# Kernel tuning notes

Hardware: AMD Instinct MI355X
Metric: run time of the kernel (lower is better)

Reference implementation:

```python
import jax, jax.numpy as jnp
import numpy as np

B, S, D, H = 4, 2048, 256, 8  # batch, seq (context=target), hidden_dim, n_heads


def setup_inputs() -> dict:
    key = jax.random.key(0)
    ks = jax.random.split(key, 12)
    sd = 1.0 / np.sqrt(D)          # torch Linear default init scale (uniform bound)
    sdo = 1.0 / np.sqrt(H * D)
    inp = {
        "k": jax.random.normal(ks[0], (B, S, D), jnp.float32),
        "v": jax.random.normal(ks[1], (B, S, D), jnp.float32),
        "q": jax.random.normal(ks[2], (B, S, D), jnp.float32),
        # Per-head projection weights, stacked over heads. Stored so y = x @ W + b.
        "Wk": jax.random.uniform(ks[3], (H, D, D), jnp.float32, -sd, sd),
        "bk": jax.random.uniform(ks[4], (H, D), jnp.float32, -sd, sd),
        "Wv": jax.random.uniform(ks[5], (H, D, D), jnp.float32, -sd, sd),
        "bv": jax.random.uniform(ks[6], (H, D), jnp.float32, -sd, sd),
        "Wq": jax.random.uniform(ks[7], (H, D, D), jnp.float32, -sd, sd),
        "bq": jax.random.uniform(ks[8], (H, D), jnp.float32, -sd, sd),
        # Final mixing Linear: input is heads interleaved as (hidden, head) flattened,
        # i.e. input index = hid * H + head (torch stack(dim=-1).view order).
        "Wo": jax.random.uniform(ks[9], (H * D, D), jnp.float32, -sdo, sdo),
        "bo": jax.random.uniform(ks[10], (D,), jnp.float32, -sdo, sdo),
    }
    return inp


def reference(k, v, q, Wk, bk, Wv, bv, Wq, bq, Wo, bo):
    # Per-head linear projections (batched over heads instead of a Python loop)
    k_ = jnp.einsum('bmd,hde->bhme', k, Wk) + bk[None, :, None, :]  # [B,H,S,D]
    v_ = jnp.einsum('bmd,hde->bhme', v, Wv) + bv[None, :, None, :]
    q_ = jnp.einsum('bnd,hde->bhne', q, Wq) + bq[None, :, None, :]
    scale = jnp.asarray(np.sqrt(D), k.dtype)
    # dot attention: scores[b,h,n,m] = <q_n, k_m> / sqrt(D); softmax over keys m
    scores = jnp.einsum('bhnd,bhmd->bhnm', q_, k_) / scale
    w = jax.nn.softmax(scores, axis=-1)
    rep = jnp.einsum('bhnm,bhmd->bhnd', w, v_)  # [B,H,S,D]
    # torch: stack(heads, dim=-1) -> [B,S,D,H], then view -> [B,S,D*H] (hid-major)
    outs = rep.transpose(0, 2, 3, 1).reshape(rep.shape[0], rep.shape[2], -1)
    return outs @ Wo + bo
```

## Files before the change

kernel.cpp:

```cpp
#include <hip/hip_runtime.h>

#define BB 4
#define SS 2048
#define DD 256
#define HH 8

typedef unsigned short u16;
typedef __attribute__((ext_vector_type(8))) short bf16x8;
typedef __attribute__((ext_vector_type(4))) float f32x4;
typedef __attribute__((ext_vector_type(16))) float f32x16;
typedef __attribute__((ext_vector_type(4))) short s16x4;

__device__ __forceinline__ f32x4 MFMA(bf16x8 a, bf16x8 b, f32x4 c) {
    return __builtin_amdgcn_mfma_f32_16x16x32_bf16(a, b, c, 0, 0, 0);
}
__device__ __forceinline__ f32x16 MFMA32(bf16x8 a, bf16x8 b, f32x16 c) {
    return __builtin_amdgcn_mfma_f32_32x32x16_bf16(a, b, c, 0, 0, 0);
}

__device__ __forceinline__ u16 f2bf_rtn(float x) {
    unsigned u = __float_as_uint(x);
    u += 0x7FFFu + ((u >> 16) & 1u);
    return (u16)(u >> 16);
}
__device__ __forceinline__ float bf2f(u16 h) {
    return __uint_as_float(((unsigned)h) << 16);
}
__device__ __forceinline__ void split2(float x, u16 &hi, u16 &lo) {
    hi = f2bf_rtn(x);
    lo = f2bf_rtn(x - bf2f(hi));
}

__device__ __forceinline__ void gl_lds16(const u16* g, u16* l) {
    __builtin_amdgcn_global_load_lds(
        (const __attribute__((address_space(1))) unsigned int*)(g),
        (__attribute__((address_space(3))) unsigned int*)(l), 16, 0, 0);
}

__global__ void prep_a(const float* __restrict__ x, u16* __restrict__ hi) {
    int r = blockIdx.x;
    int d = threadIdx.x;
    hi[(size_t)r * 256 + d] = f2bf_rtn(x[(size_t)r * 256 + d]);
}

__global__ void prep_w(const float* __restrict__ W, u16* __restrict__ Whi,
                       u16* __restrict__ Wlo) {
    int n = blockIdx.x;
    int h = n >> 8, e = n & 255;
    int d = threadIdx.x;
    float x = W[((size_t)h * 256 + d) * 256 + e];
    u16 hi, lo; split2(x, hi, lo);
    Whi[(size_t)n * 256 + d] = hi;
    Wlo[(size_t)n * 256 + d] = lo;
}

__global__ void prep_wo(const float* __restrict__ W, u16* __restrict__ Whi,
                        u16* __restrict__ Wlo) {
    int n = blockIdx.x;
    for (int k = threadIdx.x; k < 2048; k += 256) {
        int d = k & 255, h = k >> 8;
        float x = W[((size_t)(d * 8 + h)) * 256 + n];
        u16 hi, lo; split2(x, hi, lo);
        Whi[(size_t)n * 2048 + k] = hi;
        Wlo[(size_t)n * 2048 + k] = lo;
    }
}

__global__ void reduce_out(const float* __restrict__ P, const float* __restrict__ bias,
                           float* __restrict__ out) {
    const int i = blockIdx.x * 1024 + threadIdx.x * 4;
    f32x4 a = *(const f32x4*)(P + i);
    f32x4 b = *(const f32x4*)(P + 2097152 + i);
    f32x4 bv = *(const f32x4*)(bias + ((threadIdx.x * 4) & 255));
    *(f32x4*)(out + i) = (a + b) + bv;
}

template<int MODE, int AMODE, int TERMS, int BN, int LNXB, int SPLK>
__global__ __launch_bounds__(512, 2) void gemm_split(
    const u16* __restrict__ Ahi, const u16* __restrict__ Alo,
    const u16* __restrict__ Bhi, const u16* __restrict__ Blo,
    const float* __restrict__ bias,
    u16* __restrict__ Ohi,
    float* __restrict__ Of,
    int M, int N, int K, float scale)
{
    constexpr int WN = (BN == 128) ? 4 : 2;
    constexpr int WM = 8 / WN;
    constexpr int MSUB = (128 / WM) / 16;
    constexpr int NSUB = (BN / WN) / 16;
    constexpr int NPL = (TERMS == 3) ? 4 : (TERMS == 2) ? 3 : 2;
    constexpr int NBUF = SPLK ? 2 : 3;

    __shared__ u16 lds[NBUF * NPL * 4096];

    const int tid = threadIdx.x;
    const int lane = tid & 63, wave = tid >> 6;
    const int wm = wave / WN, wn = wave % WN;
    const int nwg = (int)gridDim.x >> SPLK;
    const int kc = SPLK ? (blockIdx.x >= (unsigned)nwg ? 1 : 0) : 0;
    const int b2 = SPLK ? ((int)blockIdx.x - kc * nwg) : (int)blockIdx.x;
    const int cpx = nwg >> 3;
    const int wgs = (b2 & 7) * cpx + (b2 >> 3);
    const int m0 = (wgs >> LNXB) * 128;
    const int n0 = (wgs & ((1 << LNXB) - 1)) * BN;
    const int kb = kc * (K >> SPLK);

    f32x4 acc[MSUB][NSUB];
#pragma unroll
    for (int i = 0; i < MSUB; ++i)
#pragma unroll
        for (int j = 0; j < NSUB; ++j) acc[i][j] = {0.f, 0.f, 0.f, 0.f};

    const int rho = tid >> 2;
    const int Xs = (tid & 3) << 3;
    const int ldsW = wave * 512;

#define G_ISSUE(k0v, p)                                                         \
    {   u16* Bse = lds + (p) * (NPL * 4096);                                    \
        size_t ga;                                                              \
        if (AMODE == 0)                                                         \
            ga = (size_t)(m0 + rho) * K + (k0v) + Xs;                           \
        else                                                                    \
            ga = ((size_t)((m0 >> 11) * 8 + ((k0v) >> 8)) * SS                  \
                  + (m0 & 2047) + rho) * DD + ((k0v) & 255) + Xs;               \
        gl_lds16(Ahi + ga, Bse + ldsW);                                         \
        if (TERMS == 3) gl_lds16(Alo + ga, Bse + 3 * 4096 + ldsW);              \
        if (BN == 128 || tid < 256) {                                           \
            size_t gb = (size_t)(n0 + rho) * K + (k0v) + Xs;                    \
            gl_lds16(Bhi + gb, Bse + 1 * 4096 + ldsW);                          \
            if (TERMS >= 2) gl_lds16(Blo + gb, Bse + 2 * 4096 + ldsW);          \
        }                                                                       \
    }

    const int NK = (K >> 5) >> SPLK;
    G_ISSUE(kb, 0);
    if (NBUF == 3) G_ISSUE(kb + 32, 1);

    int buf = 0;
    for (int kt = 0; kt < NK; ++kt) {
        if (NBUF == 3) {
            if (kt < NK - 1) {
                if (TERMS == 1)      { asm volatile("s_waitcnt vmcnt(2)" ::: "memory"); }
                else if (TERMS == 2) { asm volatile("s_waitcnt vmcnt(3)" ::: "memory"); }
                else {
                    if (wave < 4) { asm volatile("s_waitcnt vmcnt(4)" ::: "memory"); }
                    else          { asm volatile("s_waitcnt vmcnt(2)" ::: "memory"); }
                }
            } else {
                asm volatile("s_waitcnt vmcnt(0)" ::: "memory");
            }
        } else {
            asm volatile("s_waitcnt vmcnt(0)" ::: "memory");
        }
        __builtin_amdgcn_sched_barrier(0);
        __builtin_amdgcn_s_barrier();
        __builtin_amdgcn_sched_barrier(0);

        if (NBUF == 3) {
            if (kt + 2 < NK) {
                const int p2 = (buf + 2 >= 3) ? buf - 1 : buf + 2;
                G_ISSUE(kb + ((kt + 2) << 5), p2);
            }
        } else {
            if (kt + 1 < NK) G_ISSUE(kb + ((kt + 1) << 5), (kt + 1) & 1);
        }

        const u16* Bse = lds + buf * (NPL * 4096);
        const int g8 = (lane >> 4) << 3;
        const int rA = wm * (128 / WM), rB = wn * (BN / WN);
        bf16x8 bh[NSUB], bl[NSUB];
#pragma unroll
        for (int ns = 0; ns < NSUB; ++ns) {
            const int rb = rB + ns * 16 + (lane & 15);
            bh[ns] = *(const bf16x8*)(Bse + 1 * 4096 + rb * 32 + g8);
            if (TERMS >= 2) bl[ns] = *(const bf16x8*)(Bse + 2 * 4096 + rb * 32 + g8);
        }
#pragma unroll
        for (int ms = 0; ms < MSUB; ++ms) {
            const int ra = rA + ms * 16 + (lane & 15);
            bf16x8 ah = *(const bf16x8*)(Bse + ra * 32 + g8);
            bf16x8 al;
            if (TERMS == 3) al = *(const bf16x8*)(Bse + 3 * 4096 + ra * 32 + g8);
#pragma unroll
            for (int ns = 0; ns < NSUB; ++ns) {
                acc[ms][ns] = MFMA(ah, bh[ns], acc[ms][ns]);
                if (TERMS == 3) acc[ms][ns] = MFMA(al, bh[ns], acc[ms][ns]);
                if (TERMS >= 2) acc[ms][ns] = MFMA(ah, bl[ns], acc[ms][ns]);
            }
        }
        buf = (buf + 1 == NBUF) ? 0 : buf + 1;
    }
#undef G_ISSUE

#pragma unroll
    for (int ms = 0; ms < MSUB; ++ms)
#pragma unroll
        for (int ns = 0; ns < NSUB; ++ns)
#pragma unroll
            for (int r = 0; r < 4; ++r) {
                int row = m0 + wm * (128 / WM) + ms * 16 + (lane >> 4) * 4 + r;
                int col = n0 + wn * (BN / WN) + ns * 16 + (lane & 15);
                if (MODE == 3) {
                    Of[(size_t)kc * ((size_t)M * N) + (size_t)row * N + col] =
                        acc[ms][ns][r];
                } else {
                    float v = (acc[ms][ns][r] + bias[col]) * scale;
                    if (MODE == 2) {
                        Of[(size_t)row * N + col] = v;
                    } else {
                        int b = row >> 11, s = row & 2047, hh = col >> 8, e = col & 255;
                        size_t idx;
                        if (MODE == 0)
                            idx = ((size_t)(b * HH + hh) * SS + s) * DD + e;
                        else
                            idx = ((size_t)(b * HH + hh) * DD + e) * SS + s;
                        Ohi[idx] = f2bf_rtn(v);
                    }
                }
            }
}

__global__ __launch_bounds__(512, 2) void attn_kernel(
    const u16* __restrict__ Qhi,
    const u16* __restrict__ Khi,
    const u16* __restrict__ Vhi,
    u16* __restrict__ Rhi, u16* __restrict__ Rlo)
{
    __shared__ u16 lK[3][8192];
    __shared__ u16 lV[3][8192];

    const int tid = threadIdx.x, lane = tid & 63, wave = tid >> 6;
    const int qc = lane & 31, g2 = lane >> 5;
    const int wg = ((blockIdx.x & 7) << 5) + (blockIdx.x >> 3);
    const int bh = wg >> 3;
    const int qt = wg & 7;
    const size_t base = (size_t)bh * SS * DD;
    const int q0w = qt * 256 + wave * 32;

    bf16x8 qB[16];
#pragma unroll
    for (int ks = 0; ks < 16; ++ks)
        qB[ks] = *(const bf16x8*)(Qhi + base + (size_t)(q0w + qc) * DD + ks * 16 + g2 * 8);

    int koff[2], voff[2];
#pragma unroll
    for (int i = 0; i < 2; ++i) {
        const int s = tid + i * 512;
        const int kr = s >> 5, kX = s & 31;
        const int kap = (kr & 0x13) | ((kr & 4) << 1) | ((kr & 8) >> 1);
        koff[i] = kap * DD + ((kX ^ kr) << 3);
        const int ve = s >> 2, vXs = s & 3;
        voff[i] = ve * SS + (((vXs ^ ((ve >> 3) & 3))) << 3);
    }

    float l_part = 0.f;
    f32x16 acc[8];
#pragma unroll
    for (int ec = 0; ec < 8; ++ec) acc[ec] = {};

#define ISSUE(tt, p)                                                            \
    {   const u16* Kg = Khi + base + (size_t)(tt) * 32 * DD;                    \
        const u16* Vg = Vhi + base + (size_t)(tt) * 32;                         \
        u16* Kb = &lK[p][0]; u16* Vb = &lV[p][0];                               \
        gl_lds16(Kg + koff[0], Kb + wave * 512);                                \
        gl_lds16(Kg + koff[1], Kb + wave * 512 + 4096);                         \
        gl_lds16(Vg + voff[0], Vb + wave * 512);                                \
        gl_lds16(Vg + voff[1], Vb + wave * 512 + 4096);                         \
    }

    ISSUE(0, 0);
    ISSUE(1, 1);

    for (int t = 0; t < 64; ++t) {
        if (t < 63) { asm volatile("s_waitcnt vmcnt(4)" ::: "memory"); }
        else        { asm volatile("s_waitcnt vmcnt(0)" ::: "memory"); }
        __builtin_amdgcn_sched_barrier(0);
        __builtin_amdgcn_s_barrier();
        __builtin_amdgcn_sched_barrier(0);

        if (t + 2 < 64) ISSUE(t + 2, (t + 2) % 3);

        const u16* Kb = &lK[t % 3][0];
        const u16* Vb = &lV[t % 3][0];

        f32x16 sa = {}, sb = {};
        __builtin_amdgcn_s_setprio(1);
#pragma unroll
        for (int ks = 0; ks < 8; ++ks) {
            bf16x8 ka = *(const bf16x8*)(Kb + qc * DD + (((2 * ks + g2) ^ qc) << 3));
            bf16x8 kb2 = *(const bf16x8*)(Kb + qc * DD + (((2 * (ks + 8) + g2) ^ qc) << 3));
            sa = MFMA32(ka, qB[ks], sa);
            sb = MFMA32(kb2, qB[ks + 8], sb);
        }
        __builtin_amdgcn_s_setprio(0);

        f32x16 s = sa + sb;
#pragma unroll
        for (int n = 0; n < 16; ++n) s[n] = __builtin_amdgcn_exp2f(s[n] - 8.0f);
        float tl = 0.f;
#pragma unroll
        for (int n = 0; n < 16; ++n) tl += s[n];
        l_part += tl;

        bf16x8 p0, p1;
#pragma unroll
        for (int j = 0; j < 4; ++j) {
            unsigned a = __float_as_uint(s[2 * j]);
            unsigned b = __float_as_uint(s[2 * j + 1]);
            ((unsigned*)&p0)[j] = (a >> 16) | (b & 0xffff0000u);
            unsigned c = __float_as_uint(s[8 + 2 * j]);
            unsigned d = __float_as_uint(s[8 + 2 * j + 1]);
            ((unsigned*)&p1)[j] = (c >> 16) | (d & 0xffff0000u);
        }

        __builtin_amdgcn_s_setprio(1);
#pragma unroll
        for (int ec = 0; ec < 8; ++ec) {
            const int e = ec * 32 + qc;
            bf16x8 v0 = *(const bf16x8*)(Vb + e * 32 + (((g2 ^ ((e >> 3) & 3))) << 3));
            bf16x8 v1 = *(const bf16x8*)(Vb + e * 32 + ((((2 + g2) ^ ((e >> 3) & 3))) << 3));
            acc[ec] = MFMA32(v0, p0, acc[ec]);
            acc[ec] = MFMA32(v1, p1, acc[ec]);
        }
        __builtin_amdgcn_s_setprio(0);
    }
#undef ISSUE

    float l = l_part + __shfl_xor(l_part, 32);
    float inv = 1.0f / l;
    const size_t rowbase = ((size_t)bh * SS + q0w + qc) * DD;
#pragma unroll
    for (int ec = 0; ec < 8; ++ec)
#pragma unroll
        for (int rr = 0; rr < 4; ++rr) {
            const int e0 = ec * 32 + 8 * rr + 4 * g2;
            s16x4 hv, lv;
#pragma unroll
            for (int j = 0; j < 4; ++j) {
                u16 h2, l2; split2(acc[ec][4 * rr + j] * inv, h2, l2);
                hv[j] = (short)h2; lv[j] = (short)l2;
            }
            *(s16x4*)(Rhi + rowbase + e0) = hv;
            *(s16x4*)(Rlo + rowbase + e0) = lv;
        }
}

extern "C" void kernel_launch(void* const* d_in, const int* in_sizes, int n_in,
                              void* d_out, int out_size, void* d_ws, size_t ws_size,
                              hipStream_t stream)
{
    (void)in_sizes; (void)n_in; (void)out_size; (void)ws_size;
    const float* k_in = (const float*)d_in[0];
    const float* v_in = (const float*)d_in[1];
    const float* q_in = (const float*)d_in[2];
    const float* Wk   = (const float*)d_in[3];
    const float* bk   = (const float*)d_in[4];
    const float* Wv   = (const float*)d_in[5];
    const float* bv   = (const float*)d_in[6];
    const float* Wq   = (const float*)d_in[7];
    const float* bq   = (const float*)d_in[8];
    const float* Wo   = (const float*)d_in[9];
    const float* bo   = (const float*)d_in[10];
    float* out = (float*)d_out;

    char* p = (char*)d_ws;
    const size_t MB = 1024 * 1024;
    u16* WqH = (u16*)(p + 0 * MB);
    u16* WqL = (u16*)(p + 1 * MB);
    u16* WkH = (u16*)(p + 2 * MB);
    u16* WkL = (u16*)(p + 3 * MB);
    u16* WvH = (u16*)(p + 4 * MB);
    u16* WvL = (u16*)(p + 5 * MB);
    u16* WoH = (u16*)(p + 6 * MB);
    u16* WoL = (u16*)(p + 7 * MB);
    const size_t PB = 32 * MB;
    u16* QH  = (u16*)(p + 8 * MB);
    u16* KH  = (u16*)(p + 8 * MB + 1 * PB);
    u16* VTH = (u16*)(p + 8 * MB + 2 * PB);
    u16* RH  = (u16*)(p + 8 * MB + 3 * PB);
    u16* RL  = (u16*)(p + 8 * MB + 4 * PB);
    u16* AqH = (u16*)(p + 168 * MB);
    u16* AkH = (u16*)(p + 172 * MB);
    u16* AvH = (u16*)(p + 176 * MB);
    float* Pf = (float*)(p + 8 * MB);

    prep_a<<<dim3(8192), dim3(256), 0, stream>>>(q_in, AqH);
    prep_a<<<dim3(8192), dim3(256), 0, stream>>>(k_in, AkH);
    prep_a<<<dim3(8192), dim3(256), 0, stream>>>(v_in, AvH);
    prep_w<<<dim3(2048), dim3(256), 0, stream>>>(Wq, WqH, WqL);
    prep_w<<<dim3(2048), dim3(256), 0, stream>>>(Wk, WkH, WkL);
    prep_w<<<dim3(2048), dim3(256), 0, stream>>>(Wv, WvH, WvL);
    prep_wo<<<dim3(256), dim3(256), 0, stream>>>(Wo, WoH, WoL);

    const float qscale = 1.4426950408889634f / 16.0f;
    gemm_split<0, 0, 1, 128, 4, 0><<<dim3(1024), dim3(512), 0, stream>>>(
        AqH, nullptr, WqH, WqL, bq, QH, nullptr, 8192, 2048, 256, qscale);
    gemm_split<0, 0, 1, 128, 4, 0><<<dim3(1024), dim3(512), 0, stream>>>(
        AkH, nullptr, WkH, WkL, bk, KH, nullptr, 8192, 2048, 256, 1.0f);
    gemm_split<1, 0, 2, 128, 4, 0><<<dim3(1024), dim3(512), 0, stream>>>(
        AvH, nullptr, WvH, WvL, bv, VTH, nullptr, 8192, 2048, 256, 1.0f);

    attn_kernel<<<dim3(256), dim3(512), 0, stream>>>(
        QH, KH, VTH, RH, RL);

    gemm_split<3, 2, 3, 64, 2, 1><<<dim3(512), dim3(512), 0, stream>>>(
        RH, RL, WoH, WoL, bo, nullptr, Pf, 8192, 256, 2048, 1.0f);
    reduce_out<<<dim3(2048), dim3(256), 0, stream>>>(Pf, bo, out);
}
```

Before: 291.0 us.

## Fuse prep kernels and use 256-row M tiles for Q/K projections

New measurement: 279.0 us. -4.1%, faster.

```diff
diff --git a/kernel.cpp b/kernel.cpp
--- a/kernel.cpp
+++ b/kernel.cpp
@@ -37,21 +37,28 @@
         (__attribute__((address_space(3))) unsigned int*)(l), 16, 0, 0);
 }
 
-__global__ void prep_a(const float* __restrict__ x, u16* __restrict__ hi) {
-    int r = blockIdx.x;
-    int d = threadIdx.x;
-    hi[(size_t)r * 256 + d] = f2bf_rtn(x[(size_t)r * 256 + d]);
-}
-
-__global__ void prep_w(const float* __restrict__ W, u16* __restrict__ Whi,
-                       u16* __restrict__ Wlo) {
+__global__ void prep_a3(const float* __restrict__ q, const float* __restrict__ k,
+                        const float* __restrict__ v, u16* __restrict__ Q,
+                        u16* __restrict__ Kk, u16* __restrict__ V) {
+    const size_t i = (size_t)blockIdx.x * 256 + threadIdx.x;
+    Q[i]  = f2bf_rtn(q[i]);
+    Kk[i] = f2bf_rtn(k[i]);
+    V[i]  = f2bf_rtn(v[i]);
+}
+
+__global__ void prep_w3(const float* __restrict__ Wq, const float* __restrict__ Wk,
+                        const float* __restrict__ Wv,
+                        u16* __restrict__ QH2, u16* __restrict__ KH2,
+                        u16* __restrict__ VH2, u16* __restrict__ VL2) {
     int n = blockIdx.x;
     int h = n >> 8, e = n & 255;
     int d = threadIdx.x;
-    float x = W[((size_t)h * 256 + d) * 256 + e];
-    u16 hi, lo; split2(x, hi, lo);
-    Whi[(size_t)n * 256 + d] = hi;
-    Wlo[(size_t)n * 256 + d] = lo;
+    const size_t src = ((size_t)h * 256 + d) * 256 + e;
+    const size_t dst = (size_t)n * 256 + d;
+    QH2[dst] = f2bf_rtn(Wq[src]);
+    KH2[dst] = f2bf_rtn(Wk[src]);
+    u16 hi, lo; split2(Wv[src], hi, lo);
+    VH2[dst] = hi; VL2[dst] = lo;
 }
 
 __global__ void prep_wo(const float* __restrict__ W, u16* __restrict__ Whi,
@@ -75,7 +82,7 @@
     *(f32x4*)(out + i) = (a + b) + bv;
 }
 
-template<int MODE, int AMODE, int TERMS, int BN, int LNXB, int SPLK>
+template<int MODE, int AMODE, int TERMS, int BN, int LNXB, int SPLK, int BM>
 __global__ __launch_bounds__(512, 2) void gemm_split(
     const u16* __restrict__ Ahi, const u16* __restrict__ Alo,
     const u16* __restrict__ Bhi, const u16* __restrict__ Blo,
@@ -86,12 +93,13 @@
 {
     constexpr int WN = (BN == 128) ? 4 : 2;
     constexpr int WM = 8 / WN;
-    constexpr int MSUB = (128 / WM) / 16;
+    constexpr int MSUB = (BM / WM) / 16;
     constexpr int NSUB = (BN / WN) / 16;
-    constexpr int NPL = (TERMS == 3) ? 4 : (TERMS == 2) ? 3 : 2;
+    constexpr int ASZ = BM * 32;
+    constexpr int BUFSZ = ASZ * ((TERMS == 3) ? 2 : 1) + 4096 * ((TERMS >= 2) ? 2 : 1);
     constexpr int NBUF = SPLK ? 2 : 3;
 
-    __shared__ u16 lds[NBUF * NPL * 4096];
+    __shared__ u16 lds[NBUF * BUFSZ];
 
     const int tid = threadIdx.x;
     const int lane = tid & 63, wave = tid >> 6;
@@ -101,7 +109,7 @@
     const int b2 = SPLK ? ((int)blockIdx.x - kc * nwg) : (int)blockIdx.x;
     const int cpx = nwg >> 3;
     const int wgs = (b2 & 7) * cpx + (b2 >> 3);
-    const int m0 = (wgs >> LNXB) * 128;
+    const int m0 = (wgs >> LNXB) * BM;
     const int n0 = (wgs & ((1 << LNXB) - 1)) * BN;
     const int kb = kc * (K >> SPLK);
 
@@ -114,9 +122,10 @@
     const int rho = tid >> 2;
     const int Xs = (tid & 3) << 3;
     const int ldsW = wave * 512;
+    const size_t ga2 = (AMODE == 0) ? (size_t)128 * K : (size_t)128 * DD;
 
 #define G_ISSUE(k0v, p)                                                         \
-    {   u16* Bse = lds + (p) * (NPL * 4096);                                    \
+    {   u16* Bse = lds + (p) * BUFSZ;                                           \
         size_t ga;                                                              \
         if (AMODE == 0)                                                         \
             ga = (size_t)(m0 + rho) * K + (k0v) + Xs;                           \
@@ -124,11 +133,12 @@
             ga = ((size_t)((m0 >> 11) * 8 + ((k0v) >> 8)) * SS                  \
                   + (m0 & 2047) + rho) * DD + ((k0v) & 255) + Xs;               \
         gl_lds16(Ahi + ga, Bse + ldsW);                                         \
-        if (TERMS == 3) gl_lds16(Alo + ga, Bse + 3 * 4096 + ldsW);              \
+        if (BM == 256) gl_lds16(Ahi + ga + ga2, Bse + 4096 + ldsW);             \
+        if (TERMS == 3) gl_lds16(Alo + ga, Bse + ASZ + 8192 + ldsW);            \
         if (BN == 128 || tid < 256) {                                           \
             size_t gb = (size_t)(n0 + rho) * K + (k0v) + Xs;                    \
-            gl_lds16(Bhi + gb, Bse + 1 * 4096 + ldsW);                          \
-            if (TERMS >= 2) gl_lds16(Blo + gb, Bse + 2 * 4096 + ldsW);          \
+            gl_lds16(Bhi + gb, Bse + ASZ + ldsW);                               \
+            if (TERMS >= 2) gl_lds16(Blo + gb, Bse + ASZ + 4096 + ldsW);        \
         }                                                                       \
     }
 
@@ -140,9 +150,13 @@
     for (int kt = 0; kt < NK; ++kt) {
         if (NBUF == 3) {
             if (kt < NK - 1) {
-                if (TERMS == 1)      { asm volatile("s_waitcnt vmcnt(2)" ::: "memory"); }
-                else if (TERMS == 2) { asm volatile("s_waitcnt vmcnt(3)" ::: "memory"); }
-                else {
+                constexpr int W_HI = (BM / 128) * ((TERMS == 3) ? 2 : 1)
+                                     + ((TERMS >= 2) ? 2 : 1);
+                if (BN == 128) {
+                    if constexpr (W_HI == 2)      { asm volatile("s_waitcnt vmcnt(2)" ::: "memory"); }
+                    else if constexpr (W_HI == 3) { asm volatile("s_waitcnt vmcnt(3)" ::: "memory"); }
+                    else                          { asm volatile("s_waitcnt vmcnt(4)" ::: "memory"); }
+                } else {
                     if (wave < 4) { asm volatile("s_waitcnt vmcnt(4)" ::: "memory"); }
                     else          { asm volatile("s_waitcnt vmcnt(2)" ::: "memory"); }
                 }
@@ -165,22 +179,22 @@
             if (kt + 1 < NK) G_ISSUE(kb + ((kt + 1) << 5), (kt + 1) & 1);
         }
 
-        const u16* Bse = lds + buf * (NPL * 4096);
+        const u16* Bse = lds + buf * BUFSZ;
         const int g8 = (lane >> 4) << 3;
-        const int rA = wm * (128 / WM), rB = wn * (BN / WN);
+        const int rA = wm * (BM / WM), rB = wn * (BN / WN);
         bf16x8 bh[NSUB], bl[NSUB];
 #pragma unroll
         for (int ns = 0; ns < NSUB; ++ns) {
             const int rb = rB + ns * 16 + (lane & 15);
-            bh[ns] = *(const bf16x8*)(Bse + 1 * 4096 + rb * 32 + g8);
-            if (TERMS >= 2) bl[ns] = *(const bf16x8*)(Bse + 2 * 4096 + rb * 32 + g8);
+            bh[ns] = *(const bf16x8*)(Bse + ASZ + rb * 32 + g8);
+            if (TERMS >= 2) bl[ns] = *(const bf16x8*)(Bse + ASZ + 4096 + rb * 32 + g8);
         }
 #pragma unroll
         for (int ms = 0; ms < MSUB; ++ms) {
             const int ra = rA + ms * 16 + (lane & 15);
             bf16x8 ah = *(const bf16x8*)(Bse + ra * 32 + g8);
             bf16x8 al;
-            if (TERMS == 3) al = *(const bf16x8*)(Bse + 3 * 4096 + ra * 32 + g8);
+            if (TERMS == 3) al = *(const bf16x8*)(Bse + ASZ + 8192 + ra * 32 + g8);
 #pragma unroll
             for (int ns = 0; ns < NSUB; ++ns) {
                 acc[ms][ns] = MFMA(ah, bh[ns], acc[ms][ns]);
@@ -198,7 +212,7 @@
         for (int ns = 0; ns < NSUB; ++ns)
 #pragma unroll
             for (int r = 0; r < 4; ++r) {
-                int row = m0 + wm * (128 / WM) + ms * 16 + (lane >> 4) * 4 + r;
+                int row = m0 + wm * (BM / WM) + ms * 16 + (lane >> 4) * 4 + r;
                 int col = n0 + wn * (BN / WN) + ns * 16 + (lane & 15);
                 if (MODE == 3) {
                     Of[(size_t)kc * ((size_t)M * N) + (size_t)row * N + col] =
@@ -384,26 +398,22 @@
     u16* AvH = (u16*)(p + 176 * MB);
     float* Pf = (float*)(p + 8 * MB);
 
-    prep_a<<<dim3(8192), dim3(256), 0, stream>>>(q_in, AqH);
-    prep_a<<<dim3(8192), dim3(256), 0, stream>>>(k_in, AkH);
-    prep_a<<<dim3(8192), dim3(256), 0, stream>>>(v_in, AvH);
-    prep_w<<<dim3(2048), dim3(256), 0, stream>>>(Wq, WqH, WqL);
-    prep_w<<<dim3(2048), dim3(256), 0, stream>>>(Wk, WkH, WkL);
-    prep_w<<<dim3(2048), dim3(256), 0, stream>>>(Wv, WvH, WvL);
+    prep_a3<<<dim3(8192), dim3(256), 0, stream>>>(q_in, k_in, v_in, AqH, AkH, AvH);
+    prep_w3<<<dim3(2048), dim3(256), 0, stream>>>(Wq, Wk, Wv, WqH, WkH, WvH, WvL);
     prep_wo<<<dim3(256), dim3(256), 0, stream>>>(Wo, WoH, WoL);
 
     const float qscale = 1.4426950408889634f / 16.0f;
-    gemm_split<0, 0, 1, 128, 4, 0><<<dim3(1024), dim3(512), 0, stream>>>(
+    gemm_split<0, 0, 1, 128, 4, 0, 256><<<dim3(512), dim3(512), 0, stream>>>(
         AqH, nullptr, WqH, WqL, bq, QH, nullptr, 8192, 2048, 256, qscale);
-    gemm_split<0, 0, 1, 128, 4, 0><<<dim3(1024), dim3(512), 0, stream>>>(
+    gemm_split<0, 0, 1, 128, 4, 0, 256><<<dim3(512), dim3(512), 0, stream>>>(
         AkH, nullptr, WkH, WkL, bk, KH, nullptr, 8192, 2048, 256, 1.0f);
-    gemm_split<1, 0, 2, 128, 4, 0><<<dim3(1024), dim3(512), 0, stream>>>(
+    gemm_split<1, 0, 2, 128, 4, 0, 128><<<dim3(1024), dim3(512), 0, stream>>>(
         AvH, nullptr, WvH, WvL, bv, VTH, nullptr, 8192, 2048, 256, 1.0f);
 
     attn_kernel<<<dim3(256), dim3(512), 0, stream>>>(
         QH, KH, VTH, RH, RL);
 
-    gemm_split<3, 2, 3, 64, 2, 1><<<dim3(512), dim3(512), 0, stream>>>(
+    gemm_split<3, 2, 3, 64, 2, 1, 128><<<dim3(512), dim3(512), 0, stream>>>(
         RH, RL, WoH, WoL, bo, nullptr, Pf, 8192, 256, 2048, 1.0f);
     reduce_out<<<dim3(2048), dim3(256), 0, stream>>>(Pf, bo, out);
 }
```
